# Kernel optimization log

Measured on AMD Instinct MI355X. Metric: run time of the kernel, lower is better.

## Reference

```python
import jax, jax.numpy as jnp
import numpy as np

B, T, C = 4, 4096, 1024
H = 16            # num_heads from init_kwargs
D = C // H        # head_dim = 64
W_SCALE = 0.02    # realistic init scale for weights


def setup_inputs() -> dict:
    key = jax.random.key(0)
    ks = jax.random.split(key, 9)
    inp = {"x": jax.random.normal(ks[0], (B, T, C), dtype=jnp.float32)}
    for i, nm in enumerate(["q", "k", "v", "o"]):
        inp[f"W{nm}"] = jax.random.normal(ks[1 + i], (C, C), dtype=jnp.float32) * W_SCALE
        inp[f"b{nm}"] = jnp.zeros((C,), dtype=jnp.float32)
    return inp


def reference(x, Wq, bq, Wk, bk, Wv, bv, Wo, bo):
    Bx, Tx, Cx = x.shape
    # projections (torch Linear: y = x @ W.T + b), split heads
    q = (x @ Wq.T + bq).reshape(Bx, Tx, H, D)
    k = (x @ Wk.T + bk).reshape(Bx, Tx, H, D)
    v = (x @ Wv.T + bv).reshape(Bx, Tx, H, D)
    # ELU+1 feature map
    q = jax.nn.elu(q) + 1.0
    k = jax.nn.elu(k) + 1.0
    # global KV aggregation: kv[b,h,d,e] = sum_t k[b,t,h,d] * v[b,t,h,e]
    kv = jnp.einsum('bthd,bthe->bhde', k, v)
    # normalizer: q . (sum_t k)
    denom = jnp.einsum('bthd,bhd->bth', q, k.sum(axis=1))
    num = jnp.einsum('bthd,bhde->bthe', q, kv)
    out = num / jnp.clip(denom, 1e-6, None)[..., None]
    out = out.reshape(Bx, Tx, Cx)
    return out @ Wo.T + bo
```

## Files before the change

### kernel.cpp

```cpp
#include <hip/hip_runtime.h>
#include <hip/hip_bf16.h>
#include <stdint.h>


#define B_ 4
#define T_ 4096
#define C_ 1024
#define H_ 16
#define D_ 64
#define M_ (B_*T_)
#define TCH 512
#define K_ 1024
#define NT_ (K_/64)

using u16 = unsigned short;
using u32 = unsigned int;

typedef __attribute__((ext_vector_type(8))) short bf16x8;
typedef __attribute__((ext_vector_type(4))) float f32x4;

static __device__ __forceinline__ u16 f2bf(float f){
  u32 u = __float_as_uint(f);
  u32 r = (u + 0x7fffu + ((u >> 16) & 1u)) >> 16;
  return (u16)r;
}
static __device__ __forceinline__ void unpack8(uint4 u, float* f){
  f[0]=__uint_as_float(u.x<<16); f[1]=__uint_as_float(u.x&0xffff0000u);
  f[2]=__uint_as_float(u.y<<16); f[3]=__uint_as_float(u.y&0xffff0000u);
  f[4]=__uint_as_float(u.z<<16); f[5]=__uint_as_float(u.z&0xffff0000u);
  f[6]=__uint_as_float(u.w<<16); f[7]=__uint_as_float(u.w&0xffff0000u);
}
static __device__ __forceinline__ void gload16(const u16* g, u16* l){
  __builtin_amdgcn_global_load_lds(
      (const __attribute__((address_space(1))) void*)g,
      (__attribute__((address_space(3))) void*)l, 16, 0, 0);
}

#define FENCE() asm volatile("" ::: "memory")
#define BAR() do { FENCE(); __builtin_amdgcn_s_barrier(); FENCE(); } while(0)

__global__ __launch_bounds__(256) void cvt_all(
    const float* __restrict__ x,
    const float* __restrict__ s0, const float* __restrict__ s1,
    const float* __restrict__ s2, const float* __restrict__ s3,
    u16* __restrict__ xb,
    u16* __restrict__ d0, u16* __restrict__ d1,
    u16* __restrict__ d2, u16* __restrict__ d3)
{
  const float* s; u16* d; int bi;
  if (blockIdx.x < 8192) { s = x; d = xb; bi = blockIdx.x; }
  else {
    const int seg = (blockIdx.x - 8192) >> 9;
    bi = (blockIdx.x - 8192) & 511;
    s = seg==0?s0:seg==1?s1:seg==2?s2:s3;
    d = seg==0?d0:seg==1?d1:seg==2?d2:d3;
  }
  const int i = (bi*256 + threadIdx.x) * 8;
  const float4 a = *(const float4*)(s + i);
  const float4 b = *(const float4*)(s + i + 4);
  uint4 o;
  o.x = (u32)f2bf(a.x) | ((u32)f2bf(a.y) << 16);
  o.y = (u32)f2bf(a.z) | ((u32)f2bf(a.w) << 16);
  o.z = (u32)f2bf(b.x) | ((u32)f2bf(b.y) << 16);
  o.w = (u32)f2bf(b.z) | ((u32)f2bf(b.w) << 16);
  *(uint4*)(d + i) = o;
}

template<bool FUSED>
__global__ __launch_bounds__(1024, 4) void gemm256(
    const u16* __restrict__ X, const u16* __restrict__ Wm,
    const float* __restrict__ b0, const float* __restrict__ b1,
    const float* __restrict__ b2,
    void* __restrict__ Y0, void* __restrict__ Y1, void* __restrict__ Y2)
{
  extern __shared__ __align__(16) u16 lds[];
  const int tid  = threadIdx.x;
  const int lane = tid & 63, w = tid >> 6;
  const int wr = w >> 2, wc = w & 3;
  const int fr = lane & 15, hi = lane >> 4;

  const int xcd = blockIdx.x & 7;
  const int r   = blockIdx.x >> 3;
  const int ppx = gridDim.x >> 7;
  const int patchIdx = xcd * ppx + (r >> 4);
  const int wi = r & 15;
  const int pm = FUSED ? (patchIdx & 15) : patchIdx;
  const int pn = FUSED ? (patchIdx >> 4) : 0;
  const int bm = pm*4 + (wi & 3);
  const int bn = pn*4 + (wi >> 2);

  const int srow = tid >> 3;
  const int scc  = (tid & 7) ^ (srow & 7);
  const u16* gA = X  + (size_t)(bm*256 + srow)*K_ + scc*8;
  const u16* gB = Wm + (size_t)(bn*256 + srow)*K_ + scc*8;

  auto stageA = [&](int slot, int kt){
    const size_t ko = (size_t)kt * 64;
    gload16(gA + ko,                  lds + slot*16384 + tid*8);
    gload16(gA + (size_t)128*K_ + ko, lds + slot*16384 + 8192 + tid*8);
  };
  auto stageB = [&](int slot, int kt){
    const size_t ko = (size_t)kt * 64;
    gload16(gB + ko,                  lds + 49152 + slot*16384 + tid*8);
    gload16(gB + (size_t)128*K_ + ko, lds + 49152 + slot*16384 + 8192 + tid*8);
  };

  f32x4 acc[4][4] = {};
  const int cx0 = (hi ^ (fr & 7)) << 3;
  const int cx1 = ((4 + hi) ^ (fr & 7)) << 3;
  const u16* Abase = lds + (wr >> 1)*8192 + ((wr & 1)*64 + fr)*64;
  const u16* Bbase = lds + 49152 + (wc >> 1)*8192 + ((wc & 1)*64 + fr)*64;

  stageA(0,0); stageB(0,0);
  stageA(1,1);
  asm volatile("s_waitcnt vmcnt(2)" ::: "memory");
  BAR();

#define TILE(AS, BS, BSG, BKT, ASG, AKT, MODE) \
  { \
    bf16x8 a[4], b[4]; \
    _Pragma("unroll") \
    for (int i = 0; i < 4; ++i) a[i] = *(const bf16x8*)&Abase[(AS)*16384 + cx0 + i*1024]; \
    _Pragma("unroll") \
    for (int j = 0; j < 4; ++j) b[j] = *(const bf16x8*)&Bbase[(BS)*16384 + cx0 + j*1024]; \
    if (MODE != 2) stageB((BSG), (BKT)); \
    if (MODE == 0) stageA((ASG), (AKT)); \
    __builtin_amdgcn_sched_barrier(0); \
    __builtin_amdgcn_s_setprio(1); \
    _Pragma("unroll") \
    for (int i = 0; i < 4; ++i) \
      _Pragma("unroll") \
      for (int j = 0; j < 4; ++j) \
        acc[i][j] = __builtin_amdgcn_mfma_f32_16x16x32_bf16(a[i], b[j], acc[i][j], 0, 0, 0); \
    __builtin_amdgcn_s_setprio(0); \
    __builtin_amdgcn_sched_barrier(0); \
    _Pragma("unroll") \
    for (int i = 0; i < 4; ++i) a[i] = *(const bf16x8*)&Abase[(AS)*16384 + cx1 + i*1024]; \
    _Pragma("unroll") \
    for (int j = 0; j < 4; ++j) b[j] = *(const bf16x8*)&Bbase[(BS)*16384 + cx1 + j*1024]; \
    __builtin_amdgcn_s_setprio(1); \
    _Pragma("unroll") \
    for (int i = 0; i < 4; ++i) \
      _Pragma("unroll") \
      for (int j = 0; j < 4; ++j) \
        acc[i][j] = __builtin_amdgcn_mfma_f32_16x16x32_bf16(a[i], b[j], acc[i][j], 0, 0, 0); \
    __builtin_amdgcn_s_setprio(0); \
    if (MODE == 0)      asm volatile("s_waitcnt vmcnt(2)" ::: "memory"); \
    else if (MODE == 1) asm volatile("s_waitcnt vmcnt(0)" ::: "memory"); \
    if (MODE != 2) BAR(); \
  }

  TILE(0,0, 1, 1, 2, 2, 0)
  TILE(1,1, 0, 2, 0, 3, 0)
  TILE(2,0, 1, 3, 1, 4, 0)
  TILE(0,1, 0, 4, 2, 5, 0)
  TILE(1,0, 1, 5, 0, 6, 0)
  TILE(2,1, 0, 6, 1, 7, 0)
  TILE(0,0, 1, 7, 2, 8, 0)
  TILE(1,1, 0, 8, 0, 9, 0)
  TILE(2,0, 1, 9, 1,10, 0)
  TILE(0,1, 0,10, 2,11, 0)
  TILE(1,0, 1,11, 0,12, 0)
  TILE(2,1, 0,12, 1,13, 0)
  TILE(0,0, 1,13, 2,14, 0)
  TILE(1,1, 0,14, 0,15, 0)
  TILE(2,0, 1,15, 0, 0, 1)
  TILE(0,1, 0, 0, 0, 0, 2)

#undef TILE

  const int nloc = wc*64 + fr;
  if constexpr (FUSED) {
    const int sel  = bn >> 2;
    const int colb = (bn & 3)*256 + nloc;
    const float* bp = (sel == 0 ? b0 : sel == 1 ? b1 : b2);
    u16* Y = (u16*)(sel == 0 ? Y0 : sel == 1 ? Y1 : Y2);
    const bool elu = sel < 2;
    float bb[4];
    #pragma unroll
    for (int j = 0; j < 4; ++j) bb[j] = bp[colb + j*16];
    #pragma unroll
    for (int i = 0; i < 4; ++i) {
      #pragma unroll
      for (int r2 = 0; r2 < 4; ++r2) {
        const size_t row = (size_t)(bm*256 + wr*64 + i*16 + hi*4 + r2);
        u16* yp = Y + row*1024 + colb;
        #pragma unroll
        for (int j = 0; j < 4; ++j) {
          float vv = acc[i][j][r2] + bb[j];
          if (elu) vv = (vv > 0.0f) ? (vv + 1.0f) : __expf(vv);
          yp[j*16] = f2bf(vv);
        }
      }
    }
  } else {
    const int n0 = bn*256 + nloc;
    float bb[4];
    #pragma unroll
    for (int j = 0; j < 4; ++j) bb[j] = b0[n0 + j*16];
    float* Y = (float*)Y0;
    #pragma unroll
    for (int i = 0; i < 4; ++i) {
      #pragma unroll
      for (int r2 = 0; r2 < 4; ++r2) {
        const size_t row = (size_t)(bm*256 + wr*64 + i*16 + hi*4 + r2);
        float* yp = Y + row*1024 + n0;
        #pragma unroll
        for (int j = 0; j < 4; ++j)
          yp[j*16] = acc[i][j][r2] + bb[j];
      }
    }
  }
}

__global__ __launch_bounds__(256) void kv_partial(
    const u16* __restrict__ Kb, const u16* __restrict__ Vb,
    float* __restrict__ kvp, float* __restrict__ ksp)
{
  const int tid = threadIdx.x;
  const int bh = blockIdx.x;
  const int b = bh >> 4, h = bh & 15;
  const int chunk = blockIdx.y;
  __shared__ float kbuf[32][68];
  __shared__ float vbuf[32][68];
  float acc[4][4] = {};
  float ksl = 0.0f;
  const int d0 = (tid >> 4) << 2, e0 = (tid & 15) << 2;
  const int lrow = tid >> 3, lcol = (tid & 7) << 3;

  for (int s = 0; s < TCH/32; ++s) {
    const int t = chunk*TCH + s*32;
    {
      const size_t base = ((size_t)(b*T_ + t + lrow))*C_ + h*64 + lcol;
      const uint4 ku = *(const uint4*)(Kb + base);
      const uint4 vu = *(const uint4*)(Vb + base);
      float kf[8], vf[8];
      unpack8(ku, kf); unpack8(vu, vf);
      #pragma unroll
      for (int j = 0; j < 8; ++j) { kbuf[lrow][lcol+j] = kf[j]; vbuf[lrow][lcol+j] = vf[j]; }
    }
    __syncthreads();
    if (tid < 64) {
      #pragma unroll
      for (int tt = 0; tt < 32; ++tt) ksl += kbuf[tt][tid];
    }
    #pragma unroll
    for (int tt = 0; tt < 32; ++tt) {
      const float4 ka = *(const float4*)&kbuf[tt][d0];
      const float4 va = *(const float4*)&vbuf[tt][e0];
      const float kr[4] = {ka.x, ka.y, ka.z, ka.w};
      const float vr[4] = {va.x, va.y, va.z, va.w};
      #pragma unroll
      for (int i = 0; i < 4; ++i)
        #pragma unroll
        for (int j = 0; j < 4; ++j)
          acc[i][j] = fmaf(kr[i], vr[j], acc[i][j]);
    }
    __syncthreads();
  }

  float* dst = kvp + ((size_t)(chunk*64 + bh))*4096;
  #pragma unroll
  for (int i = 0; i < 4; ++i)
    *(float4*)&dst[(d0+i)*64 + e0] = make_float4(acc[i][0], acc[i][1], acc[i][2], acc[i][3]);
  if (tid < 64) ksp[((size_t)(chunk*64 + bh))*64 + tid] = ksl;
}

__global__ __launch_bounds__(256) void kv_reduce(
    const float* __restrict__ kvp, const float* __restrict__ ksp,
    u16* __restrict__ kvT)
{
  const int idx = blockIdx.x*256 + threadIdx.x;
  if (idx < 262144) {
    float s = 0.0f;
    #pragma unroll
    for (int c = 0; c < 8; ++c) s += kvp[(size_t)c*262144 + idx];
    const int bh = idx >> 12, d = (idx >> 6) & 63, e = idx & 63;
    kvT[(size_t)bh*5120 + e*64 + d] = f2bf(s);
  } else if (idx < 266240) {
    const int i2 = idx - 262144;
    float s = 0.0f;
    #pragma unroll
    for (int c = 0; c < 8; ++c) s += ksp[(size_t)c*4096 + i2];
    const int bh = i2 >> 6, d = i2 & 63;
    kvT[(size_t)bh*5120 + 4096 + d] = f2bf(s);
  } else if (idx < 266240 + 64*15*64) {
    const int i3 = idx - 266240;
    const int bh = i3 / 960, rd = i3 - bh*960;
    kvT[(size_t)bh*5120 + 4160 + rd] = 0;
  }
}

__global__ __launch_bounds__(256) void attn_norm_mfma(
    const u16* __restrict__ Qb, const u16* __restrict__ kvT,
    u16* __restrict__ attn)
{
  __shared__ __align__(16) u16 qs[256*64];
  const int tid = threadIdx.x;
  const int lane = tid & 63, w = tid >> 6;
  const int bh = blockIdx.x;
  const int b = bh >> 4, h = bh & 15;
  const int tt = blockIdx.y;
  const int fr = lane & 15, hi = lane >> 4;

  {
    const int srow = tid >> 3, scc = tid & 7;
    #pragma unroll
    for (int r = 0; r < 8; ++r) {
      const int row = r*32 + srow;
      const u16* src = Qb + ((size_t)(b*T_ + tt*256 + row))*C_ + h*64
                         + ((scc ^ (row & 7)) << 3);
      gload16(src, qs + tid*8 + r*2048);
    }
  }

  const u16* kvb = kvT + (size_t)bh*5120;
  bf16x8 bv[5][2];
  #pragma unroll
  for (int j = 0; j < 5; ++j) {
    const int row = (j < 4) ? (j*16 + fr) : (64 + fr);
    bv[j][0] = *(const bf16x8*)&kvb[row*64 + hi*8];
    bv[j][1] = *(const bf16x8*)&kvb[row*64 + 32 + hi*8];
  }

  __syncthreads();

  f32x4 accN[4][4] = {};
  f32x4 accD[4] = {};
  #pragma unroll
  for (int kh = 0; kh < 2; ++kh) {
    const int cx = ((kh*4 + hi) ^ (fr & 7)) << 3;
    bf16x8 a[4];
    #pragma unroll
    for (int i = 0; i < 4; ++i)
      a[i] = *(const bf16x8*)&qs[(w*64 + i*16 + fr)*64 + cx];
    #pragma unroll
    for (int i = 0; i < 4; ++i) {
      #pragma unroll
      for (int j = 0; j < 4; ++j)
        accN[i][j] = __builtin_amdgcn_mfma_f32_16x16x32_bf16(a[i], bv[j][kh], accN[i][j], 0, 0, 0);
      accD[i] = __builtin_amdgcn_mfma_f32_16x16x32_bf16(a[i], bv[4][kh], accD[i], 0, 0, 0);
    }
  }

  #pragma unroll
  for (int i = 0; i < 4; ++i) {
    #pragma unroll
    for (int r = 0; r < 4; ++r) {
      const float den = __shfl(accD[i][r], lane & 0x30);
      const float inv = 1.0f / fmaxf(den, 1e-6f);
      const size_t row = (size_t)(b*T_ + tt*256 + w*64 + i*16 + hi*4 + r);
      u16* yp = attn + row*1024 + h*64 + fr;
      #pragma unroll
      for (int j = 0; j < 4; ++j)
        yp[j*16] = f2bf(accN[i][j][r] * inv);
    }
  }
}

extern "C" void kernel_launch(void* const* d_in, const int* in_sizes, int n_in,
                              void* d_out, int out_size, void* d_ws, size_t ws_size,
                              hipStream_t stream)
{
  (void)in_sizes; (void)n_in; (void)out_size; (void)ws_size;
  const float* x  = (const float*)d_in[0];
  const float* Wq = (const float*)d_in[1];
  const float* bq = (const float*)d_in[2];
  const float* Wk = (const float*)d_in[3];
  const float* bk = (const float*)d_in[4];
  const float* Wv = (const float*)d_in[5];
  const float* bv = (const float*)d_in[6];
  const float* Wo = (const float*)d_in[7];
  const float* bo = (const float*)d_in[8];
  float* out = (float*)d_out;
  char* ws = (char*)d_ws;

  const size_t MB = 1024*1024;
  u16*   xb   = (u16*)(ws);
  u16*   wqb  = (u16*)(ws + 32*MB);
  u16*   wkb  = (u16*)(ws + 34*MB);
  u16*   wvb  = (u16*)(ws + 36*MB);
  u16*   wob  = (u16*)(ws + 38*MB);
  u16*   q    = (u16*)(ws + 40*MB);
  u16*   k    = (u16*)(ws + 72*MB);
  u16*   v    = (u16*)(ws + 104*MB);
  float* kvp  = (float*)(ws + 136*MB);
  float* ksp  = (float*)(ws + 144*MB);
  u16*   kvT  = (u16*)(ws + 144*MB + 131072);
  u16*   attn = xb;

  static bool s_attr_done = false;
  if (!s_attr_done) {
    (void)hipFuncSetAttribute(reinterpret_cast<const void*>(gemm256<true>),
                              hipFuncAttributeMaxDynamicSharedMemorySize, 163840);
    (void)hipFuncSetAttribute(reinterpret_cast<const void*>(gemm256<false>),
                              hipFuncAttributeMaxDynamicSharedMemorySize, 163840);
    s_attr_done = true;
  }

  dim3 blk(256);
  cvt_all<<<dim3(8192 + 4*512), blk, 0, stream>>>(
      x, Wq, Wk, Wv, Wo, xb, wqb, wkb, wvb, wob);

  gemm256<true><<<dim3(64*12), dim3(1024), 163840, stream>>>(
      xb, wqb, bq, bk, bv, q, k, v);

  kv_partial<<<dim3(B_*H_, T_/TCH), blk, 0, stream>>>(k, v, kvp, ksp);
  kv_reduce<<<dim3(1280), blk, 0, stream>>>(kvp, ksp, kvT);
  attn_norm_mfma<<<dim3(B_*H_, T_/256), blk, 0, stream>>>(q, kvT, attn);

  gemm256<false><<<dim3(64*4), dim3(1024), 163840, stream>>>(
      attn, wob, bo, bo, bo, out, out, out);
}
```

Before: 206.2 us.

## Use 8 waves with 128x64 per-wave tiles in the bf16 GEMM

The 256x256-tile GEMM now runs 512 threads (8 waves) instead of 1024 (16 waves). Each wave computes a 128x64 output sub-tile with 8x4 MFMA accumulators instead of 64x64. Global-to-LDS staging issues four loads per thread per operand instead of two, and the wait counts and epilogue row mapping are updated to match. The aim is more operand reuse per LDS fragment read and fewer waves contending for LDS bandwidth. The cost is doubled accumulator registers per thread, less latency hiding from wave parallelism, and more outstanding loads per thread.

```diff
diff --git a/kernel.cpp b/kernel.cpp
--- a/kernel.cpp
+++ b/kernel.cpp
@@ -67,7 +67,7 @@
 }
 
 template<bool FUSED>
-__global__ __launch_bounds__(1024, 4) void gemm256(
+__global__ __launch_bounds__(512, 2) void gemm256(
     const u16* __restrict__ X, const u16* __restrict__ Wm,
     const float* __restrict__ b0, const float* __restrict__ b1,
     const float* __restrict__ b2,
@@ -96,56 +96,66 @@
 
   auto stageA = [&](int slot, int kt){
     const size_t ko = (size_t)kt * 64;
-    gload16(gA + ko,                  lds + slot*16384 + tid*8);
-    gload16(gA + (size_t)128*K_ + ko, lds + slot*16384 + 8192 + tid*8);
+    u16* d = lds + slot*16384 + tid*8;
+    gload16(gA + ko,                  d);
+    gload16(gA + (size_t) 64*K_ + ko, d + 4096);
+    gload16(gA + (size_t)128*K_ + ko, d + 8192);
+    gload16(gA + (size_t)192*K_ + ko, d + 12288);
   };
   auto stageB = [&](int slot, int kt){
     const size_t ko = (size_t)kt * 64;
-    gload16(gB + ko,                  lds + 49152 + slot*16384 + tid*8);
-    gload16(gB + (size_t)128*K_ + ko, lds + 49152 + slot*16384 + 8192 + tid*8);
+    u16* d = lds + 49152 + slot*16384 + tid*8;
+    gload16(gB + ko,                  d);
+    gload16(gB + (size_t) 64*K_ + ko, d + 4096);
+    gload16(gB + (size_t)128*K_ + ko, d + 8192);
+    gload16(gB + (size_t)192*K_ + ko, d + 12288);
   };
 
-  f32x4 acc[4][4] = {};
+  f32x4 acc[8][4] = {};
   const int cx0 = (hi ^ (fr & 7)) << 3;
   const int cx1 = ((4 + hi) ^ (fr & 7)) << 3;
-  const u16* Abase = lds + (wr >> 1)*8192 + ((wr & 1)*64 + fr)*64;
-  const u16* Bbase = lds + 49152 + (wc >> 1)*8192 + ((wc & 1)*64 + fr)*64;
+  const u16* Abase = lds + wr*8192 + fr*64;
+  const u16* Bbase = lds + 49152 + wc*4096 + fr*64;
 
   stageA(0,0); stageB(0,0);
   stageA(1,1);
-  asm volatile("s_waitcnt vmcnt(2)" ::: "memory");
+  asm volatile("s_waitcnt vmcnt(4)" ::: "memory");
   BAR();
 
 #define TILE(AS, BS, BSG, BKT, ASG, AKT, MODE) \
   { \
-    bf16x8 a[4], b[4]; \
-    _Pragma("unroll") \
-    for (int i = 0; i < 4; ++i) a[i] = *(const bf16x8*)&Abase[(AS)*16384 + cx0 + i*1024]; \
-    _Pragma("unroll") \
-    for (int j = 0; j < 4; ++j) b[j] = *(const bf16x8*)&Bbase[(BS)*16384 + cx0 + j*1024]; \
+    bf16x8 a[8], b[4]; \
+    _Pragma("unroll") \
+    for (int i = 0; i < 8; ++i) \
+      a[i] = *(const bf16x8*)&Abase[(AS)*16384 + (i>>2)*4096 + (i&3)*1024 + cx0]; \
+    _Pragma("unroll") \
+    for (int j = 0; j < 4; ++j) \
+      b[j] = *(const bf16x8*)&Bbase[(BS)*16384 + j*1024 + cx0]; \
     if (MODE != 2) stageB((BSG), (BKT)); \
     if (MODE == 0) stageA((ASG), (AKT)); \
     __builtin_amdgcn_sched_barrier(0); \
     __builtin_amdgcn_s_setprio(1); \
     _Pragma("unroll") \
-    for (int i = 0; i < 4; ++i) \
+    for (int i = 0; i < 8; ++i) \
       _Pragma("unroll") \
       for (int j = 0; j < 4; ++j) \
         acc[i][j] = __builtin_amdgcn_mfma_f32_16x16x32_bf16(a[i], b[j], acc[i][j], 0, 0, 0); \
     __builtin_amdgcn_s_setprio(0); \
     __builtin_amdgcn_sched_barrier(0); \
     _Pragma("unroll") \
-    for (int i = 0; i < 4; ++i) a[i] = *(const bf16x8*)&Abase[(AS)*16384 + cx1 + i*1024]; \
-    _Pragma("unroll") \
-    for (int j = 0; j < 4; ++j) b[j] = *(const bf16x8*)&Bbase[(BS)*16384 + cx1 + j*1024]; \
+    for (int i = 0; i < 8; ++i) \
+      a[i] = *(const bf16x8*)&Abase[(AS)*16384 + (i>>2)*4096 + (i&3)*1024 + cx1]; \
+    _Pragma("unroll") \
+    for (int j = 0; j < 4; ++j) \
+      b[j] = *(const bf16x8*)&Bbase[(BS)*16384 + j*1024 + cx1]; \
     __builtin_amdgcn_s_setprio(1); \
     _Pragma("unroll") \
-    for (int i = 0; i < 4; ++i) \
+    for (int i = 0; i < 8; ++i) \
       _Pragma("unroll") \
       for (int j = 0; j < 4; ++j) \
         acc[i][j] = __builtin_amdgcn_mfma_f32_16x16x32_bf16(a[i], b[j], acc[i][j], 0, 0, 0); \
     __builtin_amdgcn_s_setprio(0); \
-    if (MODE == 0)      asm volatile("s_waitcnt vmcnt(2)" ::: "memory"); \
+    if (MODE == 0)      asm volatile("s_waitcnt vmcnt(4)" ::: "memory"); \
     else if (MODE == 1) asm volatile("s_waitcnt vmcnt(0)" ::: "memory"); \
     if (MODE != 2) BAR(); \
   }
@@ -180,10 +190,10 @@
     #pragma unroll
     for (int j = 0; j < 4; ++j) bb[j] = bp[colb + j*16];
     #pragma unroll
-    for (int i = 0; i < 4; ++i) {
+    for (int i = 0; i < 8; ++i) {
       #pragma unroll
       for (int r2 = 0; r2 < 4; ++r2) {
-        const size_t row = (size_t)(bm*256 + wr*64 + i*16 + hi*4 + r2);
+        const size_t row = (size_t)(bm*256 + wr*128 + i*16 + hi*4 + r2);
         u16* yp = Y + row*1024 + colb;
         #pragma unroll
         for (int j = 0; j < 4; ++j) {
@@ -200,10 +210,10 @@
     for (int j = 0; j < 4; ++j) bb[j] = b0[n0 + j*16];
     float* Y = (float*)Y0;
     #pragma unroll
-    for (int i = 0; i < 4; ++i) {
+    for (int i = 0; i < 8; ++i) {
       #pragma unroll
       for (int r2 = 0; r2 < 4; ++r2) {
-        const size_t row = (size_t)(bm*256 + wr*64 + i*16 + hi*4 + r2);
+        const size_t row = (size_t)(bm*256 + wr*128 + i*16 + hi*4 + r2);
         float* yp = Y + row*1024 + n0;
         #pragma unroll
         for (int j = 0; j < 4; ++j)
@@ -402,13 +412,13 @@
   cvt_all<<<dim3(8192 + 4*512), blk, 0, stream>>>(
       x, Wq, Wk, Wv, Wo, xb, wqb, wkb, wvb, wob);
 
-  gemm256<true><<<dim3(64*12), dim3(1024), 163840, stream>>>(
+  gemm256<true><<<dim3(64*12), dim3(512), 163840, stream>>>(
       xb, wqb, bq, bk, bv, q, k, v);
 
   kv_partial<<<dim3(B_*H_, T_/TCH), blk, 0, stream>>>(k, v, kvp, ksp);
   kv_reduce<<<dim3(1280), blk, 0, stream>>>(kvp, ksp, kvT);
   attn_norm_mfma<<<dim3(B_*H_, T_/256), blk, 0, stream>>>(q, kvT, attn);
 
-  gemm256<false><<<dim3(64*4), dim3(1024), 163840, stream>>>(
+  gemm256<false><<<dim3(64*4), dim3(512), 163840, stream>>>(
       attn, wob, bo, bo, bo, out, out, out);
 }
```

Result: slower. 211.9 us (+2.8%).
